# Kernel optimization log

Hardware: AMD Instinct MI355X
Metric: run time of the kernel (lower is better)

## Reference

```python
import jax, jax.numpy as jnp
import numpy as np

N = 13627        # n_nodes (from negative_sampling call in source)
E_EDGES = 504378 # n_edges
F_IN = 64
H1, H2, LIN_H = 300, 100, 100  # CONFIG HIDDEN_1/HIDDEN_2/LINEAR_HIDDEN


def setup_inputs() -> dict:
    key = jax.random.key(0)
    ks = jax.random.split(key, 10)
    x = jax.random.normal(ks[0], (N, F_IN), jnp.float32)
    edge_index = jax.random.randint(ks[1], (2, E_EDGES), 0, N, dtype=jnp.int64)
    neg_edge_index = jax.random.randint(ks[2], (2, E_EDGES), 0, N, dtype=jnp.int64)
    def w(k, shape):
        return jax.random.normal(k, shape, jnp.float32) * 0.05
    return dict(
        x=x, edge_index=edge_index, neg_edge_index=neg_edge_index,
        W1=w(ks[3], (2, F_IN, H1)), b1=jnp.zeros((H1,), jnp.float32),
        W2=w(ks[4], (2, H1, H2)), b2=jnp.zeros((H2,), jnp.float32),
        W3=w(ks[5], (2, H2, 1)), b3=jnp.zeros((1,), jnp.float32),
        linW1=w(ks[6], (F_IN, LIN_H)), linb1=jnp.zeros((LIN_H,), jnp.float32),
        linW2=w(ks[7], (F_IN, LIN_H)), linb2=jnp.zeros((LIN_H,), jnp.float32),
        c1=jnp.array([0.5], jnp.float32), c2=jnp.array([0.5], jnp.float32),
    )


def _cheb_norm(edge_index, n):
    # PyG ChebConv sym normalization with lambda_max=2: Lhat = L - I,
    # off-diagonal entries -deg[src]^-1/2 * deg[dst]^-1/2, diagonal 0.
    src, dst = edge_index[0], edge_index[1]
    deg = jax.ops.segment_sum(jnp.ones(src.shape, jnp.float32), src, num_segments=n)
    dinv = jnp.where(deg > 0, jax.lax.rsqrt(jnp.maximum(deg, 1.0)), 0.0)
    return -dinv[src] * dinv[dst]


def _cheb_conv(x, W, b, src, dst, norm, n):
    # K=2: out = Tx0 @ W[0] + Tx1 @ W[1] + b, with Tx1 = Lhat @ x (gather-scale-scatter)
    tx1 = jax.ops.segment_sum(norm[:, None] * x[src], dst, num_segments=n)
    return x @ W[0] + tx1 @ W[1] + b


def reference(x, edge_index, neg_edge_index, W1, b1, W2, b2, W3, b3,
              linW1, linb1, linW2, linb2, c1, c2):
    n = x.shape[0]
    src, dst = edge_index[0], edge_index[1]
    norm = _cheb_norm(edge_index, n)
    h = jax.nn.relu(_cheb_conv(x, W1, b1, src, dst, norm, n))
    x1 = jax.nn.relu(_cheb_conv(h, W2, b2, src, dst, norm, n))
    xo = x1 + jax.nn.relu(x @ linW1 + linb1)
    z = x1 + jax.nn.relu(x @ linW2 + linb2)
    pos = jax.nn.sigmoid(jnp.sum(z[edge_index[0]] * z[edge_index[1]], axis=1))
    pos_loss = -jnp.mean(jnp.log(pos + 1e-15))
    neg = jax.nn.sigmoid(jnp.sum(z[neg_edge_index[0]] * z[neg_edge_index[1]], axis=1))
    neg_loss = -jnp.mean(jnp.log(1.0 - neg + 1e-15))
    r_loss = pos_loss + neg_loss
    out = _cheb_conv(xo, W3, b3, src, dst, norm, n)
    return out, r_loss, c1, c2
```

## Files before the change

kernel.cpp:

```cpp
#include <hip/hip_runtime.h>
#include <math.h>


typedef unsigned short ushort_t;
typedef float v2f __attribute__((ext_vector_type(2)));
typedef short bf16x8 __attribute__((ext_vector_type(8)));
typedef float f32x4 __attribute__((ext_vector_type(4)));

#define GBM 64
#define GBN 64
#define GBK 32
#define LDK 72
#define HB  256
#define PACKN 6816
#define LDHB 320

__device__ inline short f2bf(float f) {
    unsigned u = __float_as_uint(f);
    u += 0x7fff + ((u >> 16) & 1);
    return (short)(u >> 16);
}
__device__ inline float bflo(unsigned w) { return __uint_as_float(w << 16); }
__device__ inline float bfhi(unsigned w) { return __uint_as_float(w & 0xffff0000u); }

__device__ inline float dot16fp8(uint4 ra, uint4 rb) {
    float dot = 0.0f;
    v2f fa, fb;
    fa = __builtin_amdgcn_cvt_pk_f32_fp8(ra.x, false);
    fb = __builtin_amdgcn_cvt_pk_f32_fp8(rb.x, false);
    dot += fa.x * fb.x + fa.y * fb.y;
    fa = __builtin_amdgcn_cvt_pk_f32_fp8(ra.x, true);
    fb = __builtin_amdgcn_cvt_pk_f32_fp8(rb.x, true);
    dot += fa.x * fb.x + fa.y * fb.y;
    fa = __builtin_amdgcn_cvt_pk_f32_fp8(ra.y, false);
    fb = __builtin_amdgcn_cvt_pk_f32_fp8(rb.y, false);
    dot += fa.x * fb.x + fa.y * fb.y;
    fa = __builtin_amdgcn_cvt_pk_f32_fp8(ra.y, true);
    fb = __builtin_amdgcn_cvt_pk_f32_fp8(rb.y, true);
    dot += fa.x * fb.x + fa.y * fb.y;
    fa = __builtin_amdgcn_cvt_pk_f32_fp8(ra.z, false);
    fb = __builtin_amdgcn_cvt_pk_f32_fp8(rb.z, false);
    dot += fa.x * fb.x + fa.y * fb.y;
    fa = __builtin_amdgcn_cvt_pk_f32_fp8(ra.z, true);
    fb = __builtin_amdgcn_cvt_pk_f32_fp8(rb.z, true);
    dot += fa.x * fb.x + fa.y * fb.y;
    fa = __builtin_amdgcn_cvt_pk_f32_fp8(ra.w, false);
    fb = __builtin_amdgcn_cvt_pk_f32_fp8(rb.w, false);
    dot += fa.x * fb.x + fa.y * fb.y;
    fa = __builtin_amdgcn_cvt_pk_f32_fp8(ra.w, true);
    fb = __builtin_amdgcn_cvt_pk_f32_fp8(rb.w, true);
    dot += fa.x * fb.x + fa.y * fb.y;
    return dot;
}

__device__ inline float loss_term(float d, int y) {
    float sg = __builtin_amdgcn_rcpf(1.0f + __expf(-d));
    return y ? __logf(1.0f - sg + 1e-15f) : __logf(sg + 1e-15f);
}

__global__ void pack_weights_kernel(const float* __restrict__ W1, const float* __restrict__ b1,
                                    const float* __restrict__ lw1, const float* __restrict__ lb1,
                                    const float* __restrict__ lw2, const float* __restrict__ lb2,
                                    const float* __restrict__ W2,
                                    ushort_t* __restrict__ BtA, float* __restrict__ ba,
                                    ushort_t* __restrict__ BtB) {
    int tid = blockIdx.x * blockDim.x + threadIdx.x;
    int stride = gridDim.x * blockDim.x;
    for (int i = tid; i < 576 * 128; i += stride) {
        int r = i >> 7, k = i & 127;
        float v = 0.0f;
        if (r < 300) v = W1[(size_t)k * 300 + r];
        else if (r >= 320 && r < 420) { if (k < 64) v = lw1[k * 100 + (r - 320)]; }
        else if (r >= 420 && r < 520) { if (k < 64) v = lw2[k * 100 + (r - 420)]; }
        BtA[i] = (ushort_t)f2bf(v);
    }
    for (int i = tid; i < 576; i += stride) {
        float v = 0.0f;
        if (i < 300) v = b1[i];
        else if (i >= 320 && i < 420) v = lb1[i - 320];
        else if (i >= 420 && i < 520) v = lb2[i - 420];
        ba[i] = v;
    }
    for (int i = tid; i < 256 * 320; i += stride) {
        int r = i / 320, k = i - r * 320;
        float v = 0.0f;
        if (k < 300 && r < 200)
            v = (r < 100) ? W2[(size_t)k * 100 + r] : W2[30000 + (size_t)k * 100 + (r - 100)];
        BtB[i] = (ushort_t)f2bf(v);
    }
}

__global__ __launch_bounds__(512) void hist_both_x_kernel(
    const int* __restrict__ ei, const float* __restrict__ x,
    int* __restrict__ degp, int* __restrict__ cntp,
    ushort_t* __restrict__ xb, int Nn, int E) {
    __shared__ int lhs[PACKN];
    __shared__ int lhd[PACKN];
    for (int i = threadIdx.x; i < PACKN; i += 512) { lhs[i] = 0; lhd[i] = 0; }
    __syncthreads();
    const int b = blockIdx.x;
    const int chunk = (E + HB - 1) / HB;
    const int e0 = b * chunk;
    const int e1 = (e0 + chunk < E) ? (e0 + chunk) : E;
    for (int e = e0 + threadIdx.x; e < e1; e += 512) {
        int s = ei[e], d = ei[E + e];
        atomicAdd(&lhs[s >> 1], 1 << ((s & 1) << 4));
        atomicAdd(&lhd[d >> 1], 1 << ((d & 1) << 4));
    }
    __syncthreads();
    int* ds = degp + (size_t)b * PACKN;
    int* cs = cntp + (size_t)b * PACKN;
    for (int i = threadIdx.x; i < PACKN; i += 512) { ds[i] = lhs[i]; cs[i] = lhd[i]; }
    const int rpb = (Nn + HB - 1) / HB;
    const int r0 = b * rpb;
    const int r1 = (r0 + rpb < Nn) ? (r0 + rpb) : Nn;
    for (int i = r0 * 64 + (int)threadIdx.x; i < r1 * 64; i += 512)
        xb[i] = (ushort_t)f2bf(x[i]);
}

__global__ void merge_kernel(const int* __restrict__ degp, const int* __restrict__ cntp,
                             ushort_t* __restrict__ off, int Nal,
                             float* __restrict__ dinv, int* __restrict__ rowptr,
                             float* __restrict__ acc, int n) {
    int tid = blockIdx.x * blockDim.x + threadIdx.x;
    if (tid == 0) {
        rowptr[0] = 0;
        acc[0] = 0.0f; acc[1] = 0.0f; acc[2] = 0.0f; acc[3] = 0.0f;
    }
    int v = tid >> 2, qq = tid & 3;
    if (v >= n) return;
    const int vh = v >> 1, sh = (v & 1) << 4;
    const int b0 = qq * (HB / 4), b1 = b0 + HB / 4;
    int dsum = 0, csum = 0;
    for (int b = b0; b < b1; ++b) {
        dsum += (degp[(size_t)b * PACKN + vh] >> sh) & 0xffff;
        csum += (cntp[(size_t)b * PACKN + vh] >> sh) & 0xffff;
    }
    int dtot = dsum;
    dtot += __shfl_xor(dtot, 1, 64);
    dtot += __shfl_xor(dtot, 2, 64);
    int inc = csum;
    int t = __shfl_up(inc, 1, 64); if (qq >= 1) inc += t;
    t = __shfl_up(inc, 2, 64);     if (qq >= 2) inc += t;
    int ex = inc - csum;
    if (qq == 0) dinv[v] = (dtot > 0) ? (1.0f / sqrtf((float)dtot)) : 0.0f;
    if (qq == 3) rowptr[v + 1] = inc;
    int run = ex;
    for (int b = b0; b < b1; ++b) {
        off[(size_t)b * Nal + v] = (ushort_t)run;
        run += (cntp[(size_t)b * PACKN + vh] >> sh) & 0xffff;
    }
}

__global__ void scan_kernel(int* __restrict__ rowptr, int n) {
    __shared__ int wsum[16];
    __shared__ int carry_s;
    if (threadIdx.x == 0) carry_s = 0;
    __syncthreads();
    int nchunk = (n + 1023) / 1024;
    int wid = threadIdx.x >> 6, lane = threadIdx.x & 63;
    for (int c = 0; c < nchunk; ++c) {
        int i = c * 1024 + threadIdx.x;
        int v = (i < n) ? rowptr[i + 1] : 0;
        int s = v;
        for (int off = 1; off < 64; off <<= 1) {
            int t = __shfl_up(s, off, 64);
            if (lane >= off) s += t;
        }
        if (lane == 63) wsum[wid] = s;
        __syncthreads();
        if (wid == 0 && lane < 16) {
            int wsv = wsum[lane];
            for (int off = 1; off < 16; off <<= 1) {
                int t = __shfl_up(wsv, off, 64);
                if (lane >= off) wsv += t;
            }
            wsum[lane] = wsv;
        }
        __syncthreads();
        int base = carry_s + (wid > 0 ? wsum[wid - 1] : 0);
        int inc = base + s;
        if (i < n) rowptr[i + 1] = inc;
        __syncthreads();
        if (threadIdx.x == 1023) carry_s = inc;
        __syncthreads();
    }
}

__global__ __launch_bounds__(512) void fill_lds_kernel(
    const int* __restrict__ ei, const float* __restrict__ dinv,
    const int* __restrict__ rowptr, const ushort_t* __restrict__ off, int Nal,
    int* __restrict__ colidx, float* __restrict__ wnorm, int E) {
    __shared__ int lh[PACKN];
    for (int i = threadIdx.x; i < PACKN; i += 512) lh[i] = 0;
    __syncthreads();
    const int b = blockIdx.x;
    const int chunk = (E + HB - 1) / HB;
    const int e0 = b * chunk;
    const int e1 = (e0 + chunk < E) ? (e0 + chunk) : E;
    const ushort_t* boff = off + (size_t)b * Nal;
    for (int e = e0 + threadIdx.x; e < e1; e += 512) {
        int s = ei[e], d = ei[E + e];
        int sh = (d & 1) << 4;
        int old = atomicAdd(&lh[d >> 1], 1 << sh);
        int rank = (old >> sh) & 0xffff;
        int slot = rowptr[d] + (int)boff[d] + rank;
        colidx[slot] = s;
        wnorm[slot] = -dinv[s] * dinv[d];
    }
}

__global__ void xt_kernel(const ushort_t* __restrict__ xb, const int* __restrict__ rowptr,
                          const int* __restrict__ colidx, const float* __restrict__ wnorm,
                          ushort_t* __restrict__ XTb, int n) {
    int node = (blockIdx.x * blockDim.x + threadIdx.x) >> 6;
    if (node >= n) return;
    int lane = threadIdx.x & 63;
    int grp = lane >> 4;
    int l = lane & 15;
    int j0 = rowptr[node], j1 = rowptr[node + 1];
    float a0 = 0, a1 = 0, a2 = 0, a3 = 0;
    int j = j0 + grp;
    if (j < j1) {
        float w = wnorm[j];
        int c = colidx[j];
        uint2 r = ((const uint2*)(xb + (size_t)c * 64))[l];
        for (;;) {
            int jn = j + 4;
            bool more = jn < j1;
            float wn = 0.0f;
            uint2 rn = r;
            if (more) {
                int cn = colidx[jn];
                wn = wnorm[jn];
                rn = ((const uint2*)(xb + (size_t)cn * 64))[l];
            }
            a0 += w * bflo(r.x); a1 += w * bfhi(r.x);
            a2 += w * bflo(r.y); a3 += w * bfhi(r.y);
            if (!more) break;
            j = jn; w = wn; r = rn;
        }
    }
    a0 += __shfl_xor(a0, 16, 64); a0 += __shfl_xor(a0, 32, 64);
    a1 += __shfl_xor(a1, 16, 64); a1 += __shfl_xor(a1, 32, 64);
    a2 += __shfl_xor(a2, 16, 64); a2 += __shfl_xor(a2, 32, 64);
    a3 += __shfl_xor(a3, 16, 64); a3 += __shfl_xor(a3, 32, 64);
    if (grp == 0) {
        uint2 xv = ((const uint2*)(xb + (size_t)node * 64))[l];
        *(uint2*)&XTb[(size_t)node * 128 + l * 4] = xv;
        uint2 p;
        p.x = (unsigned)(unsigned short)f2bf(a0) | ((unsigned)(unsigned short)f2bf(a1) << 16);
        p.y = (unsigned)(unsigned short)f2bf(a2) | ((unsigned)(unsigned short)f2bf(a3) << 16);
        *(uint2*)&XTb[(size_t)node * 128 + 64 + l * 4] = p;
    }
}

__global__ __launch_bounds__(256) void gemm_mfma(
    const ushort_t* __restrict__ Abf, int lda,
    const ushort_t* __restrict__ Bt, int ldbt,
    const float* __restrict__ bias,
    float* __restrict__ C, int ldc, ushort_t* __restrict__ Cbf, int ldcbf,
    int mode, int split, int Nrows, int K, int Ncols) {
    __shared__ short As[GBM * LDK];
    __shared__ short Bs[GBN * LDK];
    const int bm = blockIdx.y * GBM, bn = blockIdx.x * GBN;
    const int tid = threadIdx.x;
    const int w = tid >> 6, l = tid & 63;
    const int wm = (w >> 1) * 32, wn = (w & 1) * 32;
    const int lr = l & 15, kg = l >> 4;
    const int arow = tid >> 2, aseg = tid & 3;
    const int bcol = tid & 63, bseg = tid >> 6;
    const int arowg = bm + arow;
    const ushort_t* asrc = Abf + (size_t)arowg * lda + aseg * 8;
    const ushort_t* bsrc = Bt + (size_t)(bn + bcol) * ldbt + bseg * 8;
    const bool arow_ok = (arowg < Nrows);

    f32x4 acc00 = {0,0,0,0}, acc01 = {0,0,0,0}, acc10 = {0,0,0,0}, acc11 = {0,0,0,0};

    for (int k0 = 0; k0 < K; k0 += GBK) {
        bf16x8 va = {0,0,0,0,0,0,0,0};
        if (arow_ok) va = *(const bf16x8*)(asrc + k0);
        *(bf16x8*)&As[arow * LDK + aseg * 8] = va;
        *(bf16x8*)&Bs[bcol * LDK + bseg * 8] = *(const bf16x8*)(bsrc + k0);
        __syncthreads();
        bf16x8 a0 = *(const bf16x8*)&As[(wm + lr) * LDK + kg * 8];
        bf16x8 a1 = *(const bf16x8*)&As[(wm + 16 + lr) * LDK + kg * 8];
        bf16x8 b0 = *(const bf16x8*)&Bs[(wn + lr) * LDK + kg * 8];
        bf16x8 b1 = *(const bf16x8*)&Bs[(wn + 16 + lr) * LDK + kg * 8];
        acc00 = __builtin_amdgcn_mfma_f32_16x16x32_bf16(a0, b0, acc00, 0, 0, 0);
        acc01 = __builtin_amdgcn_mfma_f32_16x16x32_bf16(a0, b1, acc01, 0, 0, 0);
        acc10 = __builtin_amdgcn_mfma_f32_16x16x32_bf16(a1, b0, acc10, 0, 0, 0);
        acc11 = __builtin_amdgcn_mfma_f32_16x16x32_bf16(a1, b1, acc11, 0, 0, 0);
        __syncthreads();
    }
#pragma unroll
    for (int i = 0; i < 2; ++i) {
        int rbase = bm + wm + i * 16 + kg * 4;
#pragma unroll
        for (int j = 0; j < 2; ++j) {
            int col = bn + wn + j * 16 + lr;
            if (col >= Ncols) continue;
            float bv = bias ? bias[col] : 0.0f;
            f32x4 a = (i == 0) ? (j == 0 ? acc00 : acc01) : (j == 0 ? acc10 : acc11);
#pragma unroll
            for (int r = 0; r < 4; ++r) {
                int row = rbase + r;
                if (row >= Nrows) continue;
                float o = a[r] + bv;
                if (mode == 3) {
                    if (col < split)
                        Cbf[(size_t)row * ldcbf + col] = (ushort_t)f2bf(fmaxf(o, 0.0f));
                    else
                        C[(size_t)row * ldc + (col - split)] = o;
                } else {
                    if (col < split)
                        C[(size_t)row * ldc + col] = o;
                    else
                        Cbf[(size_t)row * 128 + (col - split)] = (ushort_t)f2bf(o);
                }
            }
        }
    }
}

__global__ void segsum_combine1_kernel(const ushort_t* __restrict__ hwb,
                                       const int* __restrict__ rowptr, const int* __restrict__ colidx,
                                       const float* __restrict__ wnorm,
                                       const float* __restrict__ G2a, const float* __restrict__ b2,
                                       float* __restrict__ x1, int n) {
    int node = (blockIdx.x * blockDim.x + threadIdx.x) >> 6;
    if (node >= n) return;
    int lane = threadIdx.x & 63;
    int grp = lane >> 4;
    int l = lane & 15;
    int j0 = rowptr[node], j1 = rowptr[node + 1];
    float acc[8] = {};
    int j = j0 + grp;
    if (j < j1) {
        float w = wnorm[j];
        int c = colidx[j];
        uint4 r = ((const uint4*)(hwb + (size_t)c * 128))[l];
        for (;;) {
            int jn = j + 4;
            bool more = jn < j1;
            float wn = 0.0f;
            uint4 rn = r;
            if (more) {
                int cn = colidx[jn];
                wn = wnorm[jn];
                rn = ((const uint4*)(hwb + (size_t)cn * 128))[l];
            }
            acc[0] += w * bflo(r.x); acc[1] += w * bfhi(r.x);
            acc[2] += w * bflo(r.y); acc[3] += w * bfhi(r.y);
            acc[4] += w * bflo(r.z); acc[5] += w * bfhi(r.z);
            acc[6] += w * bflo(r.w); acc[7] += w * bfhi(r.w);
            if (!more) break;
            j = jn; w = wn; r = rn;
        }
    }
#pragma unroll
    for (int k = 0; k < 8; ++k) {
        acc[k] += __shfl_xor(acc[k], 16, 64);
        acc[k] += __shfl_xor(acc[k], 32, 64);
    }
    if (grp == 0) {
        int f = l * 8;
        if (f < 100) {
            float4 g0 = *(const float4*)&G2a[(size_t)node * 100 + f];
            float4 bv0 = *(const float4*)&b2[f];
            float4 o0;
            o0.x = fmaxf(g0.x + acc[0] + bv0.x, 0.0f);
            o0.y = fmaxf(g0.y + acc[1] + bv0.y, 0.0f);
            o0.z = fmaxf(g0.z + acc[2] + bv0.z, 0.0f);
            o0.w = fmaxf(g0.w + acc[3] + bv0.w, 0.0f);
            *(float4*)&x1[(size_t)node * 100 + f] = o0;
            if (f + 8 <= 100) {
                float4 g1 = *(const float4*)&G2a[(size_t)node * 100 + f + 4];
                float4 bv1 = *(const float4*)&b2[f + 4];
                float4 o1;
                o1.x = fmaxf(g1.x + acc[4] + bv1.x, 0.0f);
                o1.y = fmaxf(g1.y + acc[5] + bv1.y, 0.0f);
                o1.z = fmaxf(g1.z + acc[6] + bv1.z, 0.0f);
                o1.w = fmaxf(g1.w + acc[7] + bv1.w, 0.0f);
                *(float4*)&x1[(size_t)node * 100 + f + 4] = o1;
            }
        }
    }
}

__global__ void combine2_kernel(const float* __restrict__ S, const float* __restrict__ x1,
                                const float* __restrict__ w3b,
                                float* __restrict__ xo, unsigned* __restrict__ zf,
                                float* __restrict__ sv, int n) {
    int idx = blockIdx.x * blockDim.x + threadIdx.x;
    if (idx >= n * 32) return;
    int i = idx >> 5, q = idx & 31;
    unsigned w = 0u;
    float part = 0.0f;
    if (q < 25) {
        float4 s1 = *(const float4*)&S[(size_t)i * 200 + q * 4];
        float4 s2 = *(const float4*)&S[(size_t)i * 200 + 100 + q * 4];
        float4 xv = *(const float4*)&x1[(size_t)i * 100 + q * 4];
        float4 a, b;
        a.x = xv.x + fmaxf(s1.x, 0.0f); a.y = xv.y + fmaxf(s1.y, 0.0f);
        a.z = xv.z + fmaxf(s1.z, 0.0f); a.w = xv.w + fmaxf(s1.w, 0.0f);
        b.x = xv.x + fmaxf(s2.x, 0.0f); b.y = xv.y + fmaxf(s2.y, 0.0f);
        b.z = xv.z + fmaxf(s2.z, 0.0f); b.w = xv.w + fmaxf(s2.w, 0.0f);
        *(float4*)&xo[(size_t)i * 100 + q * 4] = a;
        w = (unsigned)__builtin_amdgcn_cvt_pk_fp8_f32(b.x, b.y, 0, false);
        w = (unsigned)__builtin_amdgcn_cvt_pk_fp8_f32(b.z, b.w, (int)w, true);
        float4 wv = *(const float4*)&w3b[q * 4];
        part = a.x * wv.x + a.y * wv.y + a.z * wv.z + a.w * wv.w;
    }
    zf[(size_t)i * 32 + q] = w;
#pragma unroll
    for (int off = 16; off > 0; off >>= 1)
        part += __shfl_xor(part, off, 32);
    if (q == 0) sv[i] = part;
}

__global__ __launch_bounds__(256) void edge_loss_fp8_kernel(
    const unsigned* __restrict__ zf, const int* __restrict__ ei,
    const int* __restrict__ nei, int E, float* __restrict__ accv) {
    const int y = blockIdx.y;
    const int* __restrict__ lst = y ? nei : ei;
    const int l = threadIdx.x & 7;
    const int g = (blockIdx.x * blockDim.x + threadIdx.x) >> 3;
    const int ng = (gridDim.x * blockDim.x) >> 3;
    const int stride2 = 2 * ng;
    float s = 0.0f;
    const int gA = g, gB = g + ng;
    int niterA = (gA < E) ? ((E - 1 - gA) / stride2 + 1) : 0;
    int niterB = (gB < E) ? ((E - 1 - gB) / stride2 + 1) : 0;
    if (niterA > 0) {
        int eB0 = (gB < E) ? gB : (E - 1);
        int eA1 = (gA + stride2 < E) ? (gA + stride2) : (E - 1);
        int eB1 = (gB + stride2 < E) ? (gB + stride2) : (E - 1);
        int aA0 = lst[gA], bA0 = lst[E + gA];
        int aB0 = lst[eB0], bB0 = lst[E + eB0];
        int aA1 = lst[eA1], bA1 = lst[E + eA1];
        int aB1 = lst[eB1], bB1 = lst[E + eB1];
        uint4 raA = *(const uint4*)&zf[(size_t)aA0 * 32 + l * 4];
        uint4 rbA = *(const uint4*)&zf[(size_t)bA0 * 32 + l * 4];
        uint4 raB = *(const uint4*)&zf[(size_t)aB0 * 32 + l * 4];
        uint4 rbB = *(const uint4*)&zf[(size_t)bB0 * 32 + l * 4];
        for (int t = 0; t < niterA; ++t) {
            int eA2 = gA + (t + 2) * stride2; eA2 = (eA2 < E) ? eA2 : (E - 1);
            int eB2 = gB + (t + 2) * stride2; eB2 = (eB2 < E) ? eB2 : (E - 1);
            int aA2 = lst[eA2], bA2 = lst[E + eA2];
            int aB2 = lst[eB2], bB2 = lst[E + eB2];
            uint4 raA1 = *(const uint4*)&zf[(size_t)aA1 * 32 + l * 4];
            uint4 rbA1 = *(const uint4*)&zf[(size_t)bA1 * 32 + l * 4];
            uint4 raB1 = *(const uint4*)&zf[(size_t)aB1 * 32 + l * 4];
            uint4 rbB1 = *(const uint4*)&zf[(size_t)bB1 * 32 + l * 4];
            float dA = dot16fp8(raA, rbA);
            float dB = dot16fp8(raB, rbB);
            dA += __shfl_xor(dA, 1, 8); dB += __shfl_xor(dB, 1, 8);
            dA += __shfl_xor(dA, 2, 8); dB += __shfl_xor(dB, 2, 8);
            dA += __shfl_xor(dA, 4, 8); dB += __shfl_xor(dB, 4, 8);
            if (l == 0) {
                s += loss_term(dA, y);
                if (t < niterB) s += loss_term(dB, y);
            }
            aA1 = aA2; bA1 = bA2; aB1 = aB2; bB1 = bB2;
            raA = raA1; rbA = rbA1; raB = raB1; rbB = rbB1;
        }
    }
    __shared__ float red[256];
    red[threadIdx.x] = s;
    __syncthreads();
    for (int st = 128; st > 0; st >>= 1) {
        if (threadIdx.x < st) red[threadIdx.x] += red[threadIdx.x + st];
        __syncthreads();
    }
    if (threadIdx.x == 0) atomicAdd(&accv[y], red[0]);
}

__global__ void out_finalize_kernel(const float* __restrict__ xo, const float* __restrict__ W3,
                                    const float* __restrict__ b3, const int* __restrict__ rowptr,
                                    const int* __restrict__ colidx, const float* __restrict__ wnorm,
                                    const float* __restrict__ sv, const float* __restrict__ accv,
                                    const float* __restrict__ c1, const float* __restrict__ c2,
                                    float* __restrict__ out, int n, int E) {
    int i = blockIdx.x * blockDim.x + threadIdx.x;
    if (i == 0) {
        out[n]     = -(accv[0] + accv[1]) / (float)E;
        out[n + 1] = c1[0];
        out[n + 2] = c2[0];
    }
    if (i >= n) return;
    const float4* a = (const float4*)(xo + (size_t)i * 100);
    const float4* wv = (const float4*)W3;
    float acc = b3[0];
#pragma unroll
    for (int q = 0; q < 25; ++q) {
        float4 va = a[q], vw = wv[q];
        acc += va.x * vw.x + va.y * vw.y + va.z * vw.z + va.w * vw.w;
    }
    int j1 = rowptr[i + 1];
    for (int j = rowptr[i]; j < j1; ++j)
        acc += wnorm[j] * sv[colidx[j]];
    out[i] = acc;
}

extern "C" void kernel_launch(void* const* d_in, const int* in_sizes, int n_in,
                              void* d_out, int out_size, void* d_ws, size_t ws_size,
                              hipStream_t stream) {
    (void)n_in; (void)out_size; (void)ws_size;
    const float* x   = (const float*)d_in[0];
    const int*   ei  = (const int*)d_in[1];
    const int*   nei = (const int*)d_in[2];
    const float* W1  = (const float*)d_in[3];
    const float* b1  = (const float*)d_in[4];
    const float* W2  = (const float*)d_in[5];
    const float* b2  = (const float*)d_in[6];
    const float* W3  = (const float*)d_in[7];
    const float* b3  = (const float*)d_in[8];
    const float* lw1 = (const float*)d_in[9];
    const float* lb1 = (const float*)d_in[10];
    const float* lw2 = (const float*)d_in[11];
    const float* lb2 = (const float*)d_in[12];
    const float* c1  = (const float*)d_in[13];
    const float* c2  = (const float*)d_in[14];

    const int Nn = in_sizes[0] / 64;
    const int E  = in_sizes[1] / 2;

    const size_t Nal = ((size_t)Nn + 5) & ~(size_t)3;
    const size_t Eal = ((size_t)E + 3) & ~(size_t)3;

    float* ws       = (float*)d_ws;
    float* acc      = ws;
    float* dinv     = acc + 4;
    int*   rowptr   = (int*)(dinv + Nal);
    int*   colidx   = rowptr + Nal;
    float* wnorm    = (float*)(colidx + Eal);
    int*   degp     = (int*)(wnorm + Eal);
    int*   cntp     = degp + (size_t)HB * PACKN;
    ushort_t* offus = (ushort_t*)(cntp + (size_t)HB * PACKN);
    ushort_t* xb    = offus + (size_t)HB * Nal;
    ushort_t* XTb   = xb + (size_t)Nn * 64;
    ushort_t* hb    = XTb + (size_t)Nn * 128;
    ushort_t* BtA   = hb + (size_t)Nn * LDHB;
    ushort_t* BtB   = BtA + 576 * 128;
    float* ba       = (float*)(BtB + 256 * 320);
    float* G2a      = ba + 576;
    float* x1       = G2a + (size_t)Nn * 100;
    float* xo       = x1 + (size_t)Nn * 100;
    float* S        = xo + (size_t)Nn * 100;
    size_t zoff     = (size_t)(S + (size_t)Nn * 200 - ws);
    zoff = (zoff + 31) & ~(size_t)31;
    unsigned* zf    = (unsigned*)(ws + zoff);
    size_t hoff2    = zoff + (size_t)Nn * 32 + 63;
    hoff2 &= ~(size_t)63;
    ushort_t* hWb   = (ushort_t*)(ws + hoff2);
    float* sv       = ws + hoff2 + (size_t)Nn * 64;
    const int MB = (Nn + GBM - 1) / GBM;

    pack_weights_kernel<<<256, 256, 0, stream>>>(W1, b1, lw1, lb1, lw2, lb2, W2,
                                                 BtA, ba, BtB);

    hist_both_x_kernel<<<HB, 512, 0, stream>>>(ei, x, degp, cntp, xb, Nn, E);
    merge_kernel<<<(4 * Nn + 255) / 256, 256, 0, stream>>>(degp, cntp, offus, (int)Nal,
                                                           dinv, rowptr, acc, Nn);
    scan_kernel<<<1, 1024, 0, stream>>>(rowptr, Nn);
    fill_lds_kernel<<<HB, 512, 0, stream>>>(ei, dinv, rowptr, offus, (int)Nal,
                                            colidx, wnorm, E);

    xt_kernel<<<(Nn + 3) / 4, 256, 0, stream>>>(xb, rowptr, colidx, wnorm, XTb, Nn);
    gemm_mfma<<<dim3(9, MB), 256, 0, stream>>>(
        XTb, 128, BtA, 128, ba, S, 200, hb, LDHB, 3, 320, Nn, 128, 520);

    gemm_mfma<<<dim3(4, MB), 256, 0, stream>>>(
        hb, LDHB, BtB, 320, nullptr, G2a, 100, hWb, 0, 1, 100, Nn, 320, 200);
    segsum_combine1_kernel<<<(Nn + 3) / 4, 256, 0, stream>>>(hWb, rowptr, colidx, wnorm,
                                                             G2a, b2, x1, Nn);

    combine2_kernel<<<(Nn * 32 + 255) / 256, 256, 0, stream>>>(S, x1, W3 + 100,
                                                               xo, zf, sv, Nn);

    edge_loss_fp8_kernel<<<dim3(1024, 2), 256, 0, stream>>>(zf, ei, nei, E, acc);

    out_finalize_kernel<<<(Nn + 255) / 256, 256, 0, stream>>>(
        xo, W3, b3, rowptr, colidx, wnorm, sv, acc, c1, c2, (float*)d_out, Nn, E);
}
```

Measured before the change: 198.2 us.

## Record per-edge ranks during histogram and replace LDS fill with streaming scatter

```diff
diff --git a/kernel.cpp b/kernel.cpp
--- a/kernel.cpp
+++ b/kernel.cpp
@@ -92,7 +92,7 @@
 
 __global__ __launch_bounds__(512) void hist_both_x_kernel(
     const int* __restrict__ ei, const float* __restrict__ x,
-    int* __restrict__ degp, int* __restrict__ cntp,
+    int* __restrict__ degp, int* __restrict__ cntp, ushort_t* __restrict__ rank16,
     ushort_t* __restrict__ xb, int Nn, int E) {
     __shared__ int lhs[PACKN];
     __shared__ int lhd[PACKN];
@@ -105,7 +105,9 @@
     for (int e = e0 + threadIdx.x; e < e1; e += 512) {
         int s = ei[e], d = ei[E + e];
         atomicAdd(&lhs[s >> 1], 1 << ((s & 1) << 4));
-        atomicAdd(&lhd[d >> 1], 1 << ((d & 1) << 4));
+        int sh = (d & 1) << 4;
+        int old = atomicAdd(&lhd[d >> 1], 1 << sh);
+        rank16[e] = (ushort_t)((old >> sh) & 0xffff);
     }
     __syncthreads();
     int* ds = degp + (size_t)b * PACKN;
@@ -187,24 +189,17 @@
     }
 }
 
-__global__ __launch_bounds__(512) void fill_lds_kernel(
-    const int* __restrict__ ei, const float* __restrict__ dinv,
-    const int* __restrict__ rowptr, const ushort_t* __restrict__ off, int Nal,
-    int* __restrict__ colidx, float* __restrict__ wnorm, int E) {
-    __shared__ int lh[PACKN];
-    for (int i = threadIdx.x; i < PACKN; i += 512) lh[i] = 0;
-    __syncthreads();
-    const int b = blockIdx.x;
+__global__ void fill_stream_kernel(const int* __restrict__ ei, const float* __restrict__ dinv,
+                                   const int* __restrict__ rowptr,
+                                   const ushort_t* __restrict__ off, int Nal,
+                                   const ushort_t* __restrict__ rank16,
+                                   int* __restrict__ colidx, float* __restrict__ wnorm, int E) {
     const int chunk = (E + HB - 1) / HB;
-    const int e0 = b * chunk;
-    const int e1 = (e0 + chunk < E) ? (e0 + chunk) : E;
-    const ushort_t* boff = off + (size_t)b * Nal;
-    for (int e = e0 + threadIdx.x; e < e1; e += 512) {
+    int stride = gridDim.x * blockDim.x;
+    for (int e = blockIdx.x * blockDim.x + threadIdx.x; e < E; e += stride) {
+        int b = e / chunk;
         int s = ei[e], d = ei[E + e];
-        int sh = (d & 1) << 4;
-        int old = atomicAdd(&lh[d >> 1], 1 << sh);
-        int rank = (old >> sh) & 0xffff;
-        int slot = rowptr[d] + (int)boff[d] + rank;
+        int slot = rowptr[d] + (int)off[(size_t)b * Nal + d] + (int)rank16[e];
         colidx[slot] = s;
         wnorm[slot] = -dinv[s] * dinv[d];
     }
@@ -458,10 +453,10 @@
             dA += __shfl_xor(dA, 1, 8); dB += __shfl_xor(dB, 1, 8);
             dA += __shfl_xor(dA, 2, 8); dB += __shfl_xor(dB, 2, 8);
             dA += __shfl_xor(dA, 4, 8); dB += __shfl_xor(dB, 4, 8);
-            if (l == 0) {
-                s += loss_term(dA, y);
-                if (t < niterB) s += loss_term(dB, y);
-            }
+            float dsel = (l == 0) ? dA : dB;
+            float term = loss_term(dsel, y);
+            bool take = (l == 0) || (l == 1 && t < niterB);
+            s += take ? term : 0.0f;
             aA1 = aA2; bA1 = bA2; aB1 = aB2; bB1 = bB2;
             raA = raA1; rbA = rbA1; raB = raB1; rbB = rbB1;
         }
@@ -538,7 +533,8 @@
     int*   degp     = (int*)(wnorm + Eal);
     int*   cntp     = degp + (size_t)HB * PACKN;
     ushort_t* offus = (ushort_t*)(cntp + (size_t)HB * PACKN);
-    ushort_t* xb    = offus + (size_t)HB * Nal;
+    ushort_t* rank16= offus + (size_t)HB * Nal;
+    ushort_t* xb    = rank16 + Eal;
     ushort_t* XTb   = xb + (size_t)Nn * 64;
     ushort_t* hb    = XTb + (size_t)Nn * 128;
     ushort_t* BtA   = hb + (size_t)Nn * LDHB;
@@ -560,12 +556,12 @@
     pack_weights_kernel<<<256, 256, 0, stream>>>(W1, b1, lw1, lb1, lw2, lb2, W2,
                                                  BtA, ba, BtB);
 
-    hist_both_x_kernel<<<HB, 512, 0, stream>>>(ei, x, degp, cntp, xb, Nn, E);
+    hist_both_x_kernel<<<HB, 512, 0, stream>>>(ei, x, degp, cntp, rank16, xb, Nn, E);
     merge_kernel<<<(4 * Nn + 255) / 256, 256, 0, stream>>>(degp, cntp, offus, (int)Nal,
                                                            dinv, rowptr, acc, Nn);
     scan_kernel<<<1, 1024, 0, stream>>>(rowptr, Nn);
-    fill_lds_kernel<<<HB, 512, 0, stream>>>(ei, dinv, rowptr, offus, (int)Nal,
-                                            colidx, wnorm, E);
+    fill_stream_kernel<<<1024, 256, 0, stream>>>(ei, dinv, rowptr, offus, (int)Nal,
+                                                 rank16, colidx, wnorm, E);
 
     xt_kernel<<<(Nn + 3) / 4, 256, 0, stream>>>(xb, rowptr, colidx, wnorm, XTb, Nn);
     gemm_mfma<<<dim3(9, MB), 256, 0, stream>>>(
```

New measurement: 203.5 us. +2.7%, slower.
